# Performance work log

Hardware: AMD Instinct MI355X
Metric: run time of the kernel (lower is better)

## Reference

```python
import jax, jax.numpy as jnp
from jax import lax
import numpy as np

N_BITS = 12
BATCH = 4_194_304


def setup_inputs() -> dict:
    key = jax.random.key(0)
    kA, kB = jax.random.split(key)
    # Binary spike inputs (0.0 / 1.0) as the SNN logic gates expect.
    A = jax.random.randint(kA, (BATCH, N_BITS), 0, 2).astype(jnp.float32)
    B = jax.random.randint(kB, (BATCH, N_BITS), 0, 2).astype(jnp.float32)
    return {"A": A, "B": B}


def reference(A, B):
    """12-bit ripple-borrow subtractor A - B using soft boolean gate algebra.

    Gate math on {0,1} spikes: XOR(a,b)=a+b-2ab, AND=ab, OR=a+b-ab, NOT=1-a.
    Bit 11 is the LSB (loop runs i=11..0), Bin defaults to 0.
    Returns (diff [..., 12], final_borrow [..., 1]).
    """

    def step(borrow, ab):  # borrow: [batch], a/b: [batch]
        a, b = ab
        t1 = a + b - 2.0 * a * b            # xor1: a ^ b
        diff = t1 + borrow - 2.0 * t1 * borrow  # xor2: t1 ^ borrow
        na = 1.0 - a                         # not a
        term1 = na * b                       # and1
        term2 = na * borrow                  # and2
        term3 = b * borrow                   # and3
        o1 = term1 + term2 - term1 * term2   # or1
        new_borrow = o1 + term3 - o1 * term3 # or2
        return new_borrow, diff

    # Reorder bits so scan walks LSB (index 11) -> MSB (index 0).
    a_seq = jnp.moveaxis(A, -1, 0)[::-1]  # [12, batch...]
    b_seq = jnp.moveaxis(B, -1, 0)[::-1]
    borrow0 = jnp.zeros_like(A[..., 0])

    borrow, diffs = lax.scan(step, borrow0, (a_seq, b_seq))
    diffs = jnp.moveaxis(diffs[::-1], 0, -1)  # back to [..., 12], index 0 = MSB
    return diffs, borrow[..., None]
```

## Files before the change

### kernel.cpp

```cpp
#include <hip/hip_runtime.h>


typedef unsigned int v4u __attribute__((ext_vector_type(4)));

__global__ __launch_bounds__(256, 8) void Subtractor12Bit_kernel(
    const v4u* __restrict__ A4,
    const v4u* __restrict__ B4,
    v4u* __restrict__ D4,
    float* __restrict__ Borrow,
    int batch)
{
    const int row = blockIdx.x * 256 + threadIdx.x;
    if (row >= batch) return;
    const int base = row * 3;

    const v4u a0 = A4[base + 0];
    const v4u a1 = A4[base + 1];
    const v4u a2 = A4[base + 2];
    const v4u b0 = B4[base + 0];
    const v4u b1 = B4[base + 1];
    const v4u b2 = B4[base + 2];

    const unsigned ua =
        (((a0[0] >> 23) & 1u) << 11) | (((a0[1] >> 23) & 1u) << 10) |
        (((a0[2] >> 23) & 1u) <<  9) | (((a0[3] >> 23) & 1u) <<  8) |
        (((a1[0] >> 23) & 1u) <<  7) | (((a1[1] >> 23) & 1u) <<  6) |
        (((a1[2] >> 23) & 1u) <<  5) | (((a1[3] >> 23) & 1u) <<  4) |
        (((a2[0] >> 23) & 1u) <<  3) | (((a2[1] >> 23) & 1u) <<  2) |
        (((a2[2] >> 23) & 1u) <<  1) | (((a2[3] >> 23) & 1u)      );
    const unsigned ub =
        (((b0[0] >> 23) & 1u) << 11) | (((b0[1] >> 23) & 1u) << 10) |
        (((b0[2] >> 23) & 1u) <<  9) | (((b0[3] >> 23) & 1u) <<  8) |
        (((b1[0] >> 23) & 1u) <<  7) | (((b1[1] >> 23) & 1u) <<  6) |
        (((b1[2] >> 23) & 1u) <<  5) | (((b1[3] >> 23) & 1u) <<  4) |
        (((b2[0] >> 23) & 1u) <<  3) | (((b2[1] >> 23) & 1u) <<  2) |
        (((b2[2] >> 23) & 1u) <<  1) | (((b2[3] >> 23) & 1u)      );

    const unsigned diff = (ua - ub) & 0xFFFu;

    __builtin_nontemporal_store((ub > ua) ? 1.0f : 0.0f, &Borrow[row]);

    const unsigned ONE = 0x3F800000u;
    v4u d0, d1, d2;
    d0[0] = ONE & (0u - ((diff >> 11) & 1u));
    d0[1] = ONE & (0u - ((diff >> 10) & 1u));
    d0[2] = ONE & (0u - ((diff >>  9) & 1u));
    d0[3] = ONE & (0u - ((diff >>  8) & 1u));
    d1[0] = ONE & (0u - ((diff >>  7) & 1u));
    d1[1] = ONE & (0u - ((diff >>  6) & 1u));
    d1[2] = ONE & (0u - ((diff >>  5) & 1u));
    d1[3] = ONE & (0u - ((diff >>  4) & 1u));
    d2[0] = ONE & (0u - ((diff >>  3) & 1u));
    d2[1] = ONE & (0u - ((diff >>  2) & 1u));
    d2[2] = ONE & (0u - ((diff >>  1) & 1u));
    d2[3] = ONE & (0u - ( diff        & 1u));

    __builtin_nontemporal_store(d0, &D4[base + 0]);
    __builtin_nontemporal_store(d1, &D4[base + 1]);
    __builtin_nontemporal_store(d2, &D4[base + 2]);
}

extern "C" void kernel_launch(void* const* d_in, const int* in_sizes, int n_in,
                              void* d_out, int out_size, void* d_ws, size_t ws_size,
                              hipStream_t stream) {
    const float* A = (const float*)d_in[0];
    const float* B = (const float*)d_in[1];
    float* out = (float*)d_out;

    const int batch = in_sizes[0] / 12;
    float* diffs = out;
    float* borrow = out + (size_t)batch * 12;

    const int grid = (batch + 255) / 256;
    Subtractor12Bit_kernel<<<grid, 256, 0, stream>>>(
        (const v4u*)A, (const v4u*)B, (v4u*)diffs, borrow, batch);
}
```

Before: 483.1 us.

## Use grid-stride persistent loop with software-prefetched next-row loads

Launches a fixed grid of 2048 blocks that stride over rows. Each thread loads the next row's inputs before computing and storing the current one, to overlap memory latency. Output stores also change from nontemporal to regular stores, which may change cache behaviour. The kernel is a memory-bound stream, so the benefit depends on whether the fixed grid keeps enough loads in flight.

```diff
diff --git a/kernel.cpp b/kernel.cpp
--- a/kernel.cpp
+++ b/kernel.cpp
@@ -2,6 +2,17 @@
 
 
 typedef unsigned int v4u __attribute__((ext_vector_type(4)));
+
+#define NBLOCKS 2048
+
+__device__ __forceinline__ unsigned pack12(v4u x0, v4u x1, v4u x2) {
+    return (((x0[0] >> 23) & 1u) << 11) | (((x0[1] >> 23) & 1u) << 10) |
+           (((x0[2] >> 23) & 1u) <<  9) | (((x0[3] >> 23) & 1u) <<  8) |
+           (((x1[0] >> 23) & 1u) <<  7) | (((x1[1] >> 23) & 1u) <<  6) |
+           (((x1[2] >> 23) & 1u) <<  5) | (((x1[3] >> 23) & 1u) <<  4) |
+           (((x2[0] >> 23) & 1u) <<  3) | (((x2[1] >> 23) & 1u) <<  2) |
+           (((x2[2] >> 23) & 1u) <<  1) | (((x2[3] >> 23) & 1u)      );
+}
 
 __global__ __launch_bounds__(256, 8) void Subtractor12Bit_kernel(
     const v4u* __restrict__ A4,
@@ -10,54 +21,52 @@
     float* __restrict__ Borrow,
     int batch)
 {
-    const int row = blockIdx.x * 256 + threadIdx.x;
-    if (row >= batch) return;
-    const int base = row * 3;
+    const int stride = NBLOCKS * 256;
+    int r = blockIdx.x * 256 + threadIdx.x;
+    if (r >= batch) return;
 
-    const v4u a0 = A4[base + 0];
-    const v4u a1 = A4[base + 1];
-    const v4u a2 = A4[base + 2];
-    const v4u b0 = B4[base + 0];
-    const v4u b1 = B4[base + 1];
-    const v4u b2 = B4[base + 2];
+    v4u a0 = A4[r * 3 + 0], a1 = A4[r * 3 + 1], a2 = A4[r * 3 + 2];
+    v4u b0 = B4[r * 3 + 0], b1 = B4[r * 3 + 1], b2 = B4[r * 3 + 2];
 
-    const unsigned ua =
-        (((a0[0] >> 23) & 1u) << 11) | (((a0[1] >> 23) & 1u) << 10) |
-        (((a0[2] >> 23) & 1u) <<  9) | (((a0[3] >> 23) & 1u) <<  8) |
-        (((a1[0] >> 23) & 1u) <<  7) | (((a1[1] >> 23) & 1u) <<  6) |
-        (((a1[2] >> 23) & 1u) <<  5) | (((a1[3] >> 23) & 1u) <<  4) |
-        (((a2[0] >> 23) & 1u) <<  3) | (((a2[1] >> 23) & 1u) <<  2) |
-        (((a2[2] >> 23) & 1u) <<  1) | (((a2[3] >> 23) & 1u)      );
-    const unsigned ub =
-        (((b0[0] >> 23) & 1u) << 11) | (((b0[1] >> 23) & 1u) << 10) |
-        (((b0[2] >> 23) & 1u) <<  9) | (((b0[3] >> 23) & 1u) <<  8) |
-        (((b1[0] >> 23) & 1u) <<  7) | (((b1[1] >> 23) & 1u) <<  6) |
-        (((b1[2] >> 23) & 1u) <<  5) | (((b1[3] >> 23) & 1u) <<  4) |
-        (((b2[0] >> 23) & 1u) <<  3) | (((b2[1] >> 23) & 1u) <<  2) |
-        (((b2[2] >> 23) & 1u) <<  1) | (((b2[3] >> 23) & 1u)      );
+    while (true) {
+        const int rn = r + stride;
+        const bool has = rn < batch;
+        v4u na0, na1, na2, nb0, nb1, nb2;
+        if (has) {
+            na0 = A4[rn * 3 + 0]; na1 = A4[rn * 3 + 1]; na2 = A4[rn * 3 + 2];
+            nb0 = B4[rn * 3 + 0]; nb1 = B4[rn * 3 + 1]; nb2 = B4[rn * 3 + 2];
+        }
 
-    const unsigned diff = (ua - ub) & 0xFFFu;
+        const unsigned ua = pack12(a0, a1, a2);
+        const unsigned ub = pack12(b0, b1, b2);
+        const unsigned diff = (ua - ub) & 0xFFFu;
 
-    __builtin_nontemporal_store((ub > ua) ? 1.0f : 0.0f, &Borrow[row]);
+        Borrow[r] = (ub > ua) ? 1.0f : 0.0f;
 
-    const unsigned ONE = 0x3F800000u;
-    v4u d0, d1, d2;
-    d0[0] = ONE & (0u - ((diff >> 11) & 1u));
-    d0[1] = ONE & (0u - ((diff >> 10) & 1u));
-    d0[2] = ONE & (0u - ((diff >>  9) & 1u));
-    d0[3] = ONE & (0u - ((diff >>  8) & 1u));
-    d1[0] = ONE & (0u - ((diff >>  7) & 1u));
-    d1[1] = ONE & (0u - ((diff >>  6) & 1u));
-    d1[2] = ONE & (0u - ((diff >>  5) & 1u));
-    d1[3] = ONE & (0u - ((diff >>  4) & 1u));
-    d2[0] = ONE & (0u - ((diff >>  3) & 1u));
-    d2[1] = ONE & (0u - ((diff >>  2) & 1u));
-    d2[2] = ONE & (0u - ((diff >>  1) & 1u));
-    d2[3] = ONE & (0u - ( diff        & 1u));
+        const unsigned ONE = 0x3F800000u;
+        v4u d0, d1, d2;
+        d0[0] = ONE & (0u - ((diff >> 11) & 1u));
+        d0[1] = ONE & (0u - ((diff >> 10) & 1u));
+        d0[2] = ONE & (0u - ((diff >>  9) & 1u));
+        d0[3] = ONE & (0u - ((diff >>  8) & 1u));
+        d1[0] = ONE & (0u - ((diff >>  7) & 1u));
+        d1[1] = ONE & (0u - ((diff >>  6) & 1u));
+        d1[2] = ONE & (0u - ((diff >>  5) & 1u));
+        d1[3] = ONE & (0u - ((diff >>  4) & 1u));
+        d2[0] = ONE & (0u - ((diff >>  3) & 1u));
+        d2[1] = ONE & (0u - ((diff >>  2) & 1u));
+        d2[2] = ONE & (0u - ((diff >>  1) & 1u));
+        d2[3] = ONE & (0u - ( diff        & 1u));
 
-    __builtin_nontemporal_store(d0, &D4[base + 0]);
-    __builtin_nontemporal_store(d1, &D4[base + 1]);
-    __builtin_nontemporal_store(d2, &D4[base + 2]);
+        D4[r * 3 + 0] = d0;
+        D4[r * 3 + 1] = d1;
+        D4[r * 3 + 2] = d2;
+
+        if (!has) break;
+        r = rn;
+        a0 = na0; a1 = na1; a2 = na2;
+        b0 = nb0; b1 = nb1; b2 = nb2;
+    }
 }
 
 extern "C" void kernel_launch(void* const* d_in, const int* in_sizes, int n_in,
@@ -71,7 +80,8 @@
     float* diffs = out;
     float* borrow = out + (size_t)batch * 12;
 
-    const int grid = (batch + 255) / 256;
+    const int maxGrid = (batch + 255) / 256;
+    const int grid = (NBLOCKS < maxGrid) ? NBLOCKS : maxGrid;
     Subtractor12Bit_kernel<<<grid, 256, 0, stream>>>(
         (const v4u*)A, (const v4u*)B, (v4u*)diffs, borrow, batch);
 }
```

Result: faster. 468.2 us (-3.1%).
